# Kernel tuning notes

Hardware: AMD Instinct MI355X
Metric: run time of the kernel (lower is better)

## Reference

```python
import jax, jax.numpy as jnp
import numpy as np

B, S, DIM = 2, 2048, 1024
N_HEAD, HEAD_DIM = 16, 64


def setup_inputs() -> dict:
    key = jax.random.key(0)
    k1, k2, k3, k4 = jax.random.split(key, 4)
    x = jax.random.normal(k1, (B, S, DIM), dtype=jnp.float32)
    # rotary table: cos/sin pairs, shape [S, head_dim//2, 2]
    half = HEAD_DIM // 2
    inv_freq = 1.0 / (10000.0 ** (jnp.arange(0, half, dtype=jnp.float32) / half))
    t = jnp.arange(S, dtype=jnp.float32)
    ang = t[:, None] * inv_freq[None, :]
    freqs_cis = jnp.stack([jnp.cos(ang), jnp.sin(ang)], axis=-1)  # [S, half, 2]
    # causal boolean mask [1,1,S,S] (True = attend)
    mask = jnp.tril(jnp.ones((S, S), dtype=bool))[None, None]
    wqkv = jax.random.normal(k2, (3 * DIM, DIM), dtype=jnp.float32) * (DIM ** -0.5)
    wo = jax.random.normal(k3, (DIM, DIM), dtype=jnp.float32) * (DIM ** -0.5)
    return {"x": x, "freqs_cis": freqs_cis, "mask": mask, "wqkv": wqkv, "wo": wo}


def apply_rotary_emb(x, freqs_cis):
    # x: [B, S, H, D]; freqs_cis: [S, D//2, 2]
    xs = x.reshape(*x.shape[:-1], -1, 2)  # [B,S,H,D//2,2]
    fc = freqs_cis[None, :, None, :, :]  # [1,S,1,D//2,2]
    xr, xi = xs[..., 0], xs[..., 1]
    cr, ci = fc[..., 0], fc[..., 1]
    out = jnp.stack([xr * cr - xi * ci, xi * cr + xr * ci], axis=-1)
    return out.reshape(x.shape)


def reference(x, freqs_cis, mask, wqkv, wo):
    bsz, seqlen, _ = x.shape
    qkv = jnp.einsum('bsd,ed->bse', x, wqkv)  # [B,S,3*dim]
    q, k, v = jnp.split(qkv, 3, axis=-1)
    q = q.reshape(bsz, seqlen, N_HEAD, HEAD_DIM)
    k = k.reshape(bsz, seqlen, N_HEAD, HEAD_DIM)
    v = v.reshape(bsz, seqlen, N_HEAD, HEAD_DIM)
    q = apply_rotary_emb(q, freqs_cis)
    k = apply_rotary_emb(k, freqs_cis)
    scale = HEAD_DIM ** -0.5
    scores = jnp.einsum('bqhd,bkhd->bhqk', q, k) * scale  # [B,H,S,S]
    scores = jnp.where(mask, scores, jnp.finfo(scores.dtype).min)
    attn = jax.nn.softmax(scores, axis=-1)
    y = jnp.einsum('bhqk,bkhd->bqhd', attn, v).reshape(bsz, seqlen, N_HEAD * HEAD_DIM)
    return jnp.einsum('bse,de->bsd', y, wo)
```

## Files before the change

kernel.cpp:

```cpp
#include <hip/hip_runtime.h>
#include <hip/hip_bf16.h>
#include <stdint.h>


typedef __attribute__((ext_vector_type(8))) __bf16 bf16x8;
typedef __attribute__((ext_vector_type(4))) float f32x4;
typedef __attribute__((ext_vector_type(16))) float f32x16;

union B8 { uint4 u; bf16x8 v; unsigned short us[8]; };

static __device__ __forceinline__ float bf2f(unsigned short u) {
  union { unsigned int ui; float f; } x; x.ui = ((unsigned int)u) << 16; return x.f;
}
static __device__ __forceinline__ unsigned short f2bf(float f) {
  union { float f; unsigned int ui; } x; x.f = f;
  unsigned int r = x.ui + 0x7fffu + ((x.ui >> 16) & 1u);
  return (unsigned short)(r >> 16);
}
static __device__ __forceinline__ unsigned int cvt_pk_bf16(float lo, float hi) {
  unsigned int r;
  asm("v_cvt_pk_bf16_f32 %0, %1, %2" : "=v"(r) : "v"(lo), "v"(hi));
  return r;
}
static __device__ __forceinline__ f32x4 mfma16(bf16x8 a, bf16x8 b, f32x4 c) {
  return __builtin_amdgcn_mfma_f32_16x16x32_bf16(a, b, c, 0, 0, 0);
}
static __device__ __forceinline__ f32x16 mfma32(bf16x8 a, bf16x8 b, f32x16 c) {
  return __builtin_amdgcn_mfma_f32_32x32x16_bf16(a, b, c, 0, 0, 0);
}
#define AS1 __attribute__((address_space(1)))
#define AS3 __attribute__((address_space(3)))
static __device__ __forceinline__ void gload_lds16(const void* g, void* l) {
  __builtin_amdgcn_global_load_lds((const AS1 unsigned int*)g,
                                   (AS3 unsigned int*)l, 16, 0, 0);
}
#define VM_WAIT(N) do { \
    asm volatile("s_waitcnt vmcnt(" #N ")" ::: "memory"); \
    __builtin_amdgcn_sched_barrier(0); } while (0)
#define SBAR() __builtin_amdgcn_s_barrier()

__global__ __launch_bounds__(256) void cvt_all_kernel(
    const float* __restrict__ x, const float* __restrict__ wqkv,
    const float* __restrict__ wo,
    unsigned short* __restrict__ xb, unsigned short* __restrict__ wqkvb,
    unsigned short* __restrict__ wob) {
  int i = blockIdx.x * 256 + threadIdx.x;
  const float* src; unsigned short* dst; int off;
  if (i < 1048576)       { src = x;    dst = xb;    off = i; }
  else if (i < 1835008)  { src = wqkv; dst = wqkvb; off = i - 1048576; }
  else                   { src = wo;   dst = wob;   off = i - 1835008; }
  float4 f = ((const float4*)src)[off];
  ushort4 u;
  u.x = f2bf(f.x); u.y = f2bf(f.y); u.z = f2bf(f.z); u.w = f2bf(f.w);
  ((ushort4*)dst)[off] = u;
}

__global__ __launch_bounds__(512) void qkv_rope_kernel(
    const unsigned short* __restrict__ xb,
    const unsigned short* __restrict__ wqkvb,
    const float* __restrict__ freqs,
    unsigned short* __restrict__ Q,
    unsigned short* __restrict__ K,
    unsigned short* __restrict__ Vt)
{
  __shared__ __align__(16) unsigned short As[2][256 * 64];
  __shared__ __align__(16) unsigned short Bs[2][192 * 64];
  const int t = threadIdx.x;
  const int lane = t & 63, wv = t >> 6;
  const int l31 = lane & 31, lh = lane >> 5;
  const int wm = wv >> 1, wn = wv & 1;
  const int blk = blockIdx.x;
  const int xcd = blk & 7, j = blk >> 3;
  const int tm = 2 * xcd + (j >> 4), tn = j & 15;
  const int m0 = tm * 256, n0 = tn * 192;

  f32x16 acc[2][3] = {};

  auto stage = [&](int bb, int k0) {
    for (int r = 0; r < 7; ++r) {
      int cid = t + 512 * r;
      if (cid < 2048) {
        int row = cid >> 3, jc = cid & 7, sc = jc ^ (row & 7);
        gload_lds16(xb + (size_t)(m0 + row) * 1024 + k0 + sc * 8,
                    (char*)As[bb] + cid * 16);
      } else {
        int c2 = cid - 2048;
        int row = c2 >> 3, jc = c2 & 7, sc = jc ^ (row & 7);
        gload_lds16(wqkvb + (size_t)(n0 + row) * 1024 + k0 + sc * 8,
                    (char*)Bs[bb] + c2 * 16);
      }
    }
  };

  auto compute = [&](const char* Ap, const char* Bp) {
    for (int kst = 0; kst < 4; ++kst) {
      const int g = kst * 2 + lh;
      bf16x8 a[2], b[3];
      for (int sm = 0; sm < 2; ++sm) {
        int ra = wm * 64 + sm * 32 + l31;
        a[sm] = *(const bf16x8*)(Ap + ra * 128 + (g ^ (ra & 7)) * 16);
      }
      for (int sn = 0; sn < 3; ++sn) {
        int rb = wn * 96 + sn * 32 + l31;
        b[sn] = *(const bf16x8*)(Bp + rb * 128 + (g ^ (rb & 7)) * 16);
      }
      for (int sm = 0; sm < 2; ++sm)
        for (int sn = 0; sn < 3; ++sn)
          acc[sm][sn] = mfma32(a[sm], b[sn], acc[sm][sn]);
    }
  };

  stage(0, 0);
  for (int t2 = 0; t2 < 16; t2 += 2) {
    stage(1, (t2 + 1) * 64);
    VM_WAIT(7);
    SBAR();
    compute((const char*)As[0], (const char*)Bs[0]);
    SBAR();
    if (t2 < 14) { stage(0, (t2 + 2) * 64); VM_WAIT(7); }
    else         { VM_WAIT(0); }
    SBAR();
    compute((const char*)As[1], (const char*)Bs[1]);
    SBAR();
  }

  char* vbuf = (char*)As + wv * 2304;
  for (int sm = 0; sm < 2; ++sm) {
    for (int sn = 0; sn < 3; ++sn) {
      const int e0 = n0 + wn * 96 + sn * 32;
      const int seg = e0 >> 10;
      const int eh0 = e0 & 1023;
      const int h = eh0 >> 6;
      const int mB = m0 + wm * 64 + sm * 32;
      const int b_ = mB >> 11, sB = mB & 2047;
      if (seg == 2) {
        for (int rp = 0; rp < 8; ++rp) {
          const int r = rp * 2;
          const int row = (r & 3) + 8 * (r >> 2) + 4 * lh;
          unsigned int u = cvt_pk_bf16(acc[sm][sn][r], acc[sm][sn][r + 1]);
          *(unsigned int*)(vbuf + l31 * 72 + row * 2) = u;
        }
        const int dbase = eh0 & 63;
        for (int rd = 0; rd < 2; ++rd) {
          const int cc = rd * 16 + (lane >> 2);
          const int sh = lane & 3;
          uint2 lo = *(const uint2*)(vbuf + cc * 72 + sh * 16);
          uint2 hi = *(const uint2*)(vbuf + cc * 72 + sh * 16 + 8);
          uint4 w; w.x = lo.x; w.y = lo.y; w.z = hi.x; w.w = hi.y;
          *(uint4*)(Vt + ((size_t)(b_ * 16 + h) * 64 + dbase + cc) * 2048
                       + sB + sh * 8) = w;
        }
      } else {
        const int d = (e0 + l31) & 63;
        for (int r = 0; r < 16; ++r) {
          const int s_ = sB + (r & 3) + 8 * (r >> 2) + 4 * lh;
          float v = acc[sm][sn][r];
          float partner = __shfl_xor(v, 1, 64);
          float2 fc = *(const float2*)(freqs + s_ * 64 + (d & ~1));
          float outv = (d & 1) ? (v * fc.x + partner * fc.y)
                               : (v * fc.x - partner * fc.y);
          unsigned short* dst = (seg == 0) ? Q : K;
          dst[((size_t)(b_ * 16 + h) * 2048 + s_) * 64 + d] = f2bf(outv);
        }
      }
    }
  }
}

struct QState {
  bf16x8 qf0, qf1;
  f32x4 o[4];
  float lp;
};

static __device__ __forceinline__ void load_q(QState& st,
    const unsigned short* Qb, int q0, int c, int quad) {
  st.qf0 = *(const bf16x8*)(Qb + (q0 + c) * 64 + quad * 8);
  st.qf1 = *(const bf16x8*)(Qb + (q0 + c) * 64 + 32 + quad * 8);
}

static __device__ __forceinline__ void attn_chunk(
    QState& st, const char* Ks, const char* Vs, unsigned short* myp,
    int c, int quad, int k0, int q0, bool diag)
{
  f32x4 sfr[4];
  __builtin_amdgcn_s_setprio(1);
  for (int kc = 0; kc < 4; ++kc) {
    const int key = kc * 16 + c;
    const int s0 = quad ^ (key & 7), s1 = (4 + quad) ^ (key & 7);
    f32x4 sacc = {};
    sacc = mfma16(*(const bf16x8*)(Ks + key * 128 + s0 * 16), st.qf0, sacc);
    sacc = mfma16(*(const bf16x8*)(Ks + key * 128 + s1 * 16), st.qf1, sacc);
    sfr[kc] = sacc;
  }
  __builtin_amdgcn_s_setprio(0);
  const int qrow = q0 + c;
  float e[4][4];
  float lsum = 0.f;
  for (int kc = 0; kc < 4; ++kc) {
    for (int i = 0; i < 4; ++i) {
      float arg = fmaf(sfr[kc][i], 0.18033688f, -20.19773057f);
      if (diag && (k0 + kc * 16 + quad * 4 + i > qrow)) arg = -1e30f;
      e[kc][i] = __builtin_amdgcn_exp2f(arg);
    }
    lsum += (e[kc][0] + e[kc][1]) + (e[kc][2] + e[kc][3]);
  }
  st.lp += lsum;
  for (int kc = 0; kc < 4; ++kc) {
    uint2 w;
    w.x = cvt_pk_bf16(e[kc][0], e[kc][1]);
    w.y = cvt_pk_bf16(e[kc][2], e[kc][3]);
    *(uint2*)(myp + c * 72 + kc * 16 + quad * 4) = w;
  }
  bf16x8 pf[2];
  pf[0] = *(const bf16x8*)(myp + c * 72 + quad * 8);
  pf[1] = *(const bf16x8*)(myp + c * 72 + 32 + quad * 8);
  __builtin_amdgcn_s_setprio(1);
  for (int ct = 0; ct < 4; ++ct) {
    const int d = ct * 16 + c;
    const int s0 = quad ^ (d & 7), s1 = (4 + quad) ^ (d & 7);
    st.o[ct] = mfma16(pf[0], *(const bf16x8*)(Vs + d * 128 + s0 * 16), st.o[ct]);
    st.o[ct] = mfma16(pf[1], *(const bf16x8*)(Vs + d * 128 + s1 * 16), st.o[ct]);
  }
  __builtin_amdgcn_s_setprio(0);
}

__global__ __launch_bounds__(256) void attn_partial_kernel(
    const unsigned short* __restrict__ Q,
    const unsigned short* __restrict__ K,
    const unsigned short* __restrict__ Vt,
    unsigned short* __restrict__ Po,
    float* __restrict__ Pl)
{
  __shared__ __align__(16) unsigned short Ks[64 * 64];
  __shared__ __align__(16) unsigned short Vs[64 * 64];
  __shared__ __align__(16) unsigned short plds[4][16 * 72];
  const int t = threadIdx.x;
  const int lane = t & 63, wv = t >> 6;
  const int c = lane & 15, quad = lane >> 4;
  const int bh = blockIdx.x & 31;
  const int rest = blockIdx.x >> 5;
  const int j = rest >> 1, half = rest & 1;
  const int qA = j * 64 + wv * 16;
  const int qB = (31 - j) * 64 + wv * 16;

  const unsigned short* Qb = Q + (size_t)bh * (2048 * 64);
  const unsigned short* Kb = K + (size_t)bh * (2048 * 64);
  const unsigned short* Vb = Vt + (size_t)bh * (64 * 2048);

  QState A = {}, Bst = {};
  load_q(A, Qb, qA, c, quad);
  load_q(Bst, Qb, qB, c, quad);

  unsigned short* myp = plds[wv];
  const int ktmax = 31 - j;

  for (int kt = half; kt <= ktmax; kt += 2) {
    const int k0 = kt * 64;
    __syncthreads();
    for (int r = 0; r < 2; ++r) {
      int cid = t + 256 * r;
      int row = cid >> 3, jc = cid & 7;
      int sc = jc ^ (row & 7);
      gload_lds16(Kb + (size_t)(k0 + row) * 64 + sc * 8, (char*)Ks + cid * 16);
      gload_lds16(Vb + (size_t)row * 2048 + k0 + sc * 8, (char*)Vs + cid * 16);
    }
    __syncthreads();
    attn_chunk(Bst, (const char*)Ks, (const char*)Vs, myp, c, quad,
               k0, qB, kt == ktmax);
    if (kt <= j)
      attn_chunk(A, (const char*)Ks, (const char*)Vs, myp, c, quad,
                 k0, qA, kt == j);
  }

  unsigned short* Poh = Po + (size_t)half * (32 * 2048 * 64) + (size_t)bh * (2048 * 64);
  float* Plh = Pl + (size_t)half * (32 * 2048) + bh * 2048;
  for (int set = 0; set < 2; ++set) {
    QState& st = set ? Bst : A;
    const int q0 = set ? qB : qA;
    float l = st.lp;
    l += __shfl_xor(l, 16, 64);
    l += __shfl_xor(l, 32, 64);
    for (int i = 0; i < 4; ++i) {
      const int s = q0 + quad * 4 + i;
      for (int ct = 0; ct < 4; ++ct)
        Poh[(size_t)s * 64 + ct * 16 + c] = f2bf(st.o[ct][i]);
    }
    if (quad == 0) Plh[q0 + c] = l;
  }
}

__global__ __launch_bounds__(256) void combine_kernel(
    const unsigned short* __restrict__ Po, const float* __restrict__ Pl,
    unsigned short* __restrict__ Yb)
{
  const int idx = blockIdx.x * 256 + threadIdx.x;
  const int bh = idx >> 14, rem = idx & 16383;
  const int s = rem >> 3, g = rem & 7;
  const size_t base = (size_t)bh * (2048 * 64) + (size_t)s * 64 + g * 8;
  B8 a, b;
  a.u = *(const uint4*)(Po + base);
  b.u = *(const uint4*)(Po + (size_t)(32 * 2048 * 64) + base);
  float l = Pl[bh * 2048 + s] + Pl[32 * 2048 + bh * 2048 + s];
  float inv = 1.0f / l;
  B8 y;
  for (int k = 0; k < 8; ++k)
    y.us[k] = f2bf((bf2f(a.us[k]) + bf2f(b.us[k])) * inv);
  const int b_ = bh >> 4, h = bh & 15;
  *(uint4*)(Yb + ((size_t)(b_ * 2048 + s)) * 1024 + h * 64 + g * 8) = y.u;
}

__global__ __launch_bounds__(256) void attn_kernel(
    const unsigned short* __restrict__ Q,
    const unsigned short* __restrict__ K,
    const unsigned short* __restrict__ Vt,
    unsigned short* __restrict__ Y)
{
  __shared__ __align__(16) unsigned short Ks[64 * 64];
  __shared__ __align__(16) unsigned short Vs[64 * 64];
  __shared__ __align__(16) unsigned short plds[4][16 * 72];
  const int t = threadIdx.x;
  const int lane = t & 63, wv = t >> 6;
  const int c = lane & 15, quad = lane >> 4;
  const int j = blockIdx.x >> 5, bh = blockIdx.x & 31;
  const int b = bh >> 4, h = bh & 15;
  const int qA = j * 64 + wv * 16;
  const int qB = (31 - j) * 64 + wv * 16;

  const unsigned short* Qb = Q + (size_t)bh * (2048 * 64);
  const unsigned short* Kb = K + (size_t)bh * (2048 * 64);
  const unsigned short* Vb = Vt + (size_t)bh * (64 * 2048);

  QState A = {}, Bst = {};
  load_q(A, Qb, qA, c, quad);
  load_q(Bst, Qb, qB, c, quad);

  const int nkt = 32 - j;
  unsigned short* myp = plds[wv];

  for (int kt = 0; kt < nkt; ++kt) {
    const int k0 = kt * 64;
    __syncthreads();
    for (int r = 0; r < 2; ++r) {
      int cid = t + 256 * r;
      int row = cid >> 3, jc = cid & 7;
      int sc = jc ^ (row & 7);
      gload_lds16(Kb + (size_t)(k0 + row) * 64 + sc * 8, (char*)Ks + cid * 16);
      gload_lds16(Vb + (size_t)row * 2048 + k0 + sc * 8, (char*)Vs + cid * 16);
    }
    __syncthreads();
    attn_chunk(Bst, (const char*)Ks, (const char*)Vs, myp, c, quad,
               k0, qB, kt == 31 - j);
    if (kt <= j)
      attn_chunk(A, (const char*)Ks, (const char*)Vs, myp, c, quad,
                 k0, qA, kt == j);
  }

  for (int set = 0; set < 2; ++set) {
    QState& st = set ? Bst : A;
    const int q0 = set ? qB : qA;
    float l = st.lp;
    l += __shfl_xor(l, 16, 64);
    l += __shfl_xor(l, 32, 64);
    for (int i = 0; i < 4; ++i) {
      float inv = 1.0f / __shfl(l, quad * 4 + i, 64);
      const int s = q0 + quad * 4 + i;
      unsigned short* dst = Y + ((size_t)(b * 2048 + s)) * 1024 + h * 64;
      for (int ct = 0; ct < 4; ++ct)
        dst[ct * 16 + c] = f2bf(st.o[ct][i] * inv);
    }
  }
}

__global__ __launch_bounds__(256) void out_proj_kernel(
    const unsigned short* __restrict__ Y,
    const unsigned short* __restrict__ wob,
    float* __restrict__ out)
{
  __shared__ __align__(16) unsigned short As[2][128 * 64];
  __shared__ __align__(16) unsigned short Bs[2][64 * 64];
  const int t = threadIdx.x;
  const int lane = t & 63, wv = t >> 6;
  const int l31 = lane & 31, lh = lane >> 5;
  const int wm = wv >> 1, wn = wv & 1;
  const int blk = blockIdx.x;
  const int tm = (blk & 7) * 4 + ((blk >> 3) & 3);
  const int tn = blk >> 5;
  const int m0 = tm * 128, n0 = tn * 64;

  f32x16 acc[2] = {};

  auto stage = [&](int bb, int k0) {
    for (int r = 0; r < 6; ++r) {
      int cid = t + 256 * r;
      if (cid < 1024) {
        int row = cid >> 3, jc = cid & 7, sc = jc ^ (row & 7);
        gload_lds16(Y + (size_t)(m0 + row) * 1024 + k0 + sc * 8,
                    (char*)As[bb] + cid * 16);
      } else {
        int c2 = cid - 1024;
        int row = c2 >> 3, jc = c2 & 7, sc = jc ^ (row & 7);
        gload_lds16(wob + (size_t)(n0 + row) * 1024 + k0 + sc * 8,
                    (char*)Bs[bb] + c2 * 16);
      }
    }
  };

  auto compute = [&](const char* Ap, const char* Bp) {
    for (int kst = 0; kst < 4; ++kst) {
      const int g = kst * 2 + lh;
      bf16x8 a[2], b;
      for (int sm = 0; sm < 2; ++sm) {
        int ra = wm * 64 + sm * 32 + l31;
        a[sm] = *(const bf16x8*)(Ap + ra * 128 + (g ^ (ra & 7)) * 16);
      }
      int rb = wn * 32 + l31;
      b = *(const bf16x8*)(Bp + rb * 128 + (g ^ (rb & 7)) * 16);
      acc[0] = mfma32(a[0], b, acc[0]);
      acc[1] = mfma32(a[1], b, acc[1]);
    }
  };

  stage(0, 0);
  for (int t2 = 0; t2 < 16; t2 += 2) {
    stage(1, (t2 + 1) * 64);
    VM_WAIT(6);
    SBAR();
    compute((const char*)As[0], (const char*)Bs[0]);
    SBAR();
    if (t2 < 14) { stage(0, (t2 + 2) * 64); VM_WAIT(6); }
    else         { VM_WAIT(0); }
    SBAR();
    compute((const char*)As[1], (const char*)Bs[1]);
    SBAR();
  }

  const int col = n0 + wn * 32 + l31;
  for (int sm = 0; sm < 2; ++sm)
    for (int r = 0; r < 16; ++r) {
      const int m = m0 + wm * 64 + sm * 32 + (r & 3) + 8 * (r >> 2) + 4 * lh;
      out[(size_t)m * 1024 + col] = acc[sm][r];
    }
}

extern "C" void kernel_launch(void* const* d_in, const int* in_sizes, int n_in,
                              void* d_out, int out_size, void* d_ws, size_t ws_size,
                              hipStream_t stream) {
  const float* x     = (const float*)d_in[0];
  const float* freqs = (const float*)d_in[1];
  const float* wqkv  = (const float*)d_in[3];
  const float* wo    = (const float*)d_in[4];
  float* out = (float*)d_out;

  const size_t BHSD = (size_t)2 * 16 * 2048 * 64;
  unsigned short* Q     = (unsigned short*)d_ws;
  unsigned short* K     = Q + BHSD;
  unsigned short* Vt    = K + BHSD;
  unsigned short* Yb    = Vt + BHSD;
  unsigned short* xb    = Yb + BHSD;
  unsigned short* wqkvb = xb + 4194304;
  unsigned short* wob   = wqkvb + 3145728;
  unsigned short* Po    = wob + 1048576;
  float*          Pl    = (float*)(Po + 2 * BHSD);

  const size_t need_fast =
      (size_t)((char*)(Pl + 2 * 32 * 2048) - (char*)d_ws);

  cvt_all_kernel<<<8192, 256, 0, stream>>>(x, wqkv, wo, xb, wqkvb, wob);
  qkv_rope_kernel<<<256, 512, 0, stream>>>(xb, wqkvb, freqs, Q, K, Vt);
  if (ws_size >= need_fast) {
    attn_partial_kernel<<<1024, 256, 0, stream>>>(Q, K, Vt, Po, Pl);
    combine_kernel<<<2048, 256, 0, stream>>>(Po, Pl, Yb);
  } else {
    attn_kernel<<<512, 256, 0, stream>>>(Q, K, Vt, Yb);
  }
  out_proj_kernel<<<512, 256, 0, stream>>>(Yb, wob, out);
}
```

Baseline: 200.9 us.

## Fuse fp32-to-bf16 conversion into GEMM staging and drop separate convert kernel

Removes the standalone conversion kernel. The QKV projection and output projection now load fp32 x, wqkv and wo directly into registers, pack them to bf16 and write them to LDS. The register-staged loads are issued before the compute of the current tile so that global latency overlaps the MFMA work. This saves one launch and the bf16 round-trip through global memory, at the cost of reading twice the bytes for weights and activations on every tile, using more registers, and giving up the direct global-to-LDS loads for those operands.

```diff
diff --git a/kernel.cpp b/kernel.cpp
--- a/kernel.cpp
+++ b/kernel.cpp
@@ -21,6 +21,12 @@
   unsigned int r;
   asm("v_cvt_pk_bf16_f32 %0, %1, %2" : "=v"(r) : "v"(lo), "v"(hi));
   return r;
+}
+static __device__ __forceinline__ uint4 pack8(float4 a, float4 b) {
+  uint4 w;
+  w.x = cvt_pk_bf16(a.x, a.y); w.y = cvt_pk_bf16(a.z, a.w);
+  w.z = cvt_pk_bf16(b.x, b.y); w.w = cvt_pk_bf16(b.z, b.w);
+  return w;
 }
 static __device__ __forceinline__ f32x4 mfma16(bf16x8 a, bf16x8 b, f32x4 c) {
   return __builtin_amdgcn_mfma_f32_16x16x32_bf16(a, b, c, 0, 0, 0);
@@ -34,30 +40,18 @@
   __builtin_amdgcn_global_load_lds((const AS1 unsigned int*)g,
                                    (AS3 unsigned int*)l, 16, 0, 0);
 }
-#define VM_WAIT(N) do { \
-    asm volatile("s_waitcnt vmcnt(" #N ")" ::: "memory"); \
+#define VM_WAIT0() do { \
+    asm volatile("s_waitcnt vmcnt(0)" ::: "memory"); \
     __builtin_amdgcn_sched_barrier(0); } while (0)
+#define LGKM_WAIT() do { \
+    asm volatile("s_waitcnt lgkmcnt(0)" ::: "memory"); \
+    __builtin_amdgcn_sched_barrier(0); } while (0)
+#define SFENCE() __builtin_amdgcn_sched_barrier(0)
 #define SBAR() __builtin_amdgcn_s_barrier()
 
-__global__ __launch_bounds__(256) void cvt_all_kernel(
-    const float* __restrict__ x, const float* __restrict__ wqkv,
-    const float* __restrict__ wo,
-    unsigned short* __restrict__ xb, unsigned short* __restrict__ wqkvb,
-    unsigned short* __restrict__ wob) {
-  int i = blockIdx.x * 256 + threadIdx.x;
-  const float* src; unsigned short* dst; int off;
-  if (i < 1048576)       { src = x;    dst = xb;    off = i; }
-  else if (i < 1835008)  { src = wqkv; dst = wqkvb; off = i - 1048576; }
-  else                   { src = wo;   dst = wob;   off = i - 1835008; }
-  float4 f = ((const float4*)src)[off];
-  ushort4 u;
-  u.x = f2bf(f.x); u.y = f2bf(f.y); u.z = f2bf(f.z); u.w = f2bf(f.w);
-  ((ushort4*)dst)[off] = u;
-}
-
 __global__ __launch_bounds__(512) void qkv_rope_kernel(
-    const unsigned short* __restrict__ xb,
-    const unsigned short* __restrict__ wqkvb,
+    const float* __restrict__ x,
+    const float* __restrict__ wqkv,
     const float* __restrict__ freqs,
     unsigned short* __restrict__ Q,
     unsigned short* __restrict__ K,
@@ -76,19 +70,30 @@
 
   f32x16 acc[2][3] = {};
 
-  auto stage = [&](int bb, int k0) {
+  auto stage_load = [&](int k0, float4* ld) {
+#pragma unroll
     for (int r = 0; r < 7; ++r) {
       int cid = t + 512 * r;
-      if (cid < 2048) {
+      const float* src;
+      if (r < 4) {
         int row = cid >> 3, jc = cid & 7, sc = jc ^ (row & 7);
-        gload_lds16(xb + (size_t)(m0 + row) * 1024 + k0 + sc * 8,
-                    (char*)As[bb] + cid * 16);
+        src = x + (size_t)(m0 + row) * 1024 + k0 + sc * 8;
       } else {
         int c2 = cid - 2048;
         int row = c2 >> 3, jc = c2 & 7, sc = jc ^ (row & 7);
-        gload_lds16(wqkvb + (size_t)(n0 + row) * 1024 + k0 + sc * 8,
-                    (char*)Bs[bb] + c2 * 16);
+        src = wqkv + (size_t)(n0 + row) * 1024 + k0 + sc * 8;
       }
+      ld[2 * r]     = ((const float4*)src)[0];
+      ld[2 * r + 1] = ((const float4*)src)[1];
+    }
+  };
+  auto stage_write = [&](int bb, const float4* ld) {
+#pragma unroll
+    for (int r = 0; r < 7; ++r) {
+      int cid = t + 512 * r;
+      char* dst = (r < 4) ? (char*)As[bb] + cid * 16
+                          : (char*)Bs[bb] + (cid - 2048) * 16;
+      *(uint4*)dst = pack8(ld[2 * r], ld[2 * r + 1]);
     }
   };
 
@@ -110,17 +115,28 @@
     }
   };
 
-  stage(0, 0);
+  float4 ld[14];
+  stage_load(0, ld);
+  VM_WAIT0();
+  stage_write(0, ld);
+  LGKM_WAIT();
+  SBAR();
   for (int t2 = 0; t2 < 16; t2 += 2) {
-    stage(1, (t2 + 1) * 64);
-    VM_WAIT(7);
+    stage_load((t2 + 1) * 64, ld);
+    SFENCE();
+    compute((const char*)As[0], (const char*)Bs[0]);
+    VM_WAIT0();
+    stage_write(1, ld);
+    LGKM_WAIT();
     SBAR();
-    compute((const char*)As[0], (const char*)Bs[0]);
-    SBAR();
-    if (t2 < 14) { stage(0, (t2 + 2) * 64); VM_WAIT(7); }
-    else         { VM_WAIT(0); }
-    SBAR();
+    if (t2 < 14) stage_load((t2 + 2) * 64, ld);
+    SFENCE();
     compute((const char*)As[1], (const char*)Bs[1]);
+    if (t2 < 14) {
+      VM_WAIT0();
+      stage_write(0, ld);
+      LGKM_WAIT();
+    }
     SBAR();
   }
 
@@ -374,7 +390,7 @@
 
 __global__ __launch_bounds__(256) void out_proj_kernel(
     const unsigned short* __restrict__ Y,
-    const unsigned short* __restrict__ wob,
+    const float* __restrict__ wo,
     float* __restrict__ out)
 {
   __shared__ __align__(16) unsigned short As[2][128 * 64];
@@ -390,19 +406,30 @@
 
   f32x16 acc[2] = {};
 
-  auto stage = [&](int bb, int k0) {
-    for (int r = 0; r < 6; ++r) {
+  auto stage_A = [&](int bb, int k0) {
+#pragma unroll
+    for (int r = 0; r < 4; ++r) {
       int cid = t + 256 * r;
-      if (cid < 1024) {
-        int row = cid >> 3, jc = cid & 7, sc = jc ^ (row & 7);
-        gload_lds16(Y + (size_t)(m0 + row) * 1024 + k0 + sc * 8,
-                    (char*)As[bb] + cid * 16);
-      } else {
-        int c2 = cid - 1024;
-        int row = c2 >> 3, jc = c2 & 7, sc = jc ^ (row & 7);
-        gload_lds16(wob + (size_t)(n0 + row) * 1024 + k0 + sc * 8,
-                    (char*)Bs[bb] + c2 * 16);
-      }
+      int row = cid >> 3, jc = cid & 7, sc = jc ^ (row & 7);
+      gload_lds16(Y + (size_t)(m0 + row) * 1024 + k0 + sc * 8,
+                  (char*)As[bb] + cid * 16);
+    }
+  };
+  auto stage_loadB = [&](int k0, float4* lb) {
+#pragma unroll
+    for (int r = 0; r < 2; ++r) {
+      int cid = t + 256 * r;
+      int row = cid >> 3, jc = cid & 7, sc = jc ^ (row & 7);
+      const float* src = wo + (size_t)(n0 + row) * 1024 + k0 + sc * 8;
+      lb[2 * r]     = ((const float4*)src)[0];
+      lb[2 * r + 1] = ((const float4*)src)[1];
+    }
+  };
+  auto stage_writeB = [&](int bb, const float4* lb) {
+#pragma unroll
+    for (int r = 0; r < 2; ++r) {
+      int cid = t + 256 * r;
+      *(uint4*)((char*)Bs[bb] + cid * 16) = pack8(lb[2 * r], lb[2 * r + 1]);
     }
   };
 
@@ -421,17 +448,30 @@
     }
   };
 
-  stage(0, 0);
+  float4 lb[4];
+  stage_A(0, 0);
+  stage_loadB(0, lb);
+  VM_WAIT0();
+  stage_writeB(0, lb);
+  LGKM_WAIT();
+  SBAR();
   for (int t2 = 0; t2 < 16; t2 += 2) {
-    stage(1, (t2 + 1) * 64);
-    VM_WAIT(6);
+    stage_A(1, (t2 + 1) * 64);
+    stage_loadB((t2 + 1) * 64, lb);
+    SFENCE();
+    compute((const char*)As[0], (const char*)Bs[0]);
+    VM_WAIT0();
+    stage_writeB(1, lb);
+    LGKM_WAIT();
     SBAR();
-    compute((const char*)As[0], (const char*)Bs[0]);
-    SBAR();
-    if (t2 < 14) { stage(0, (t2 + 2) * 64); VM_WAIT(6); }
-    else         { VM_WAIT(0); }
-    SBAR();
+    if (t2 < 14) { stage_A(0, (t2 + 2) * 64); stage_loadB((t2 + 2) * 64, lb); }
+    SFENCE();
     compute((const char*)As[1], (const char*)Bs[1]);
+    if (t2 < 14) {
+      VM_WAIT0();
+      stage_writeB(0, lb);
+      LGKM_WAIT();
+    }
     SBAR();
   }
 
@@ -466,13 +506,12 @@
   const size_t need_fast =
       (size_t)((char*)(Pl + 2 * 32 * 2048) - (char*)d_ws);
 
-  cvt_all_kernel<<<8192, 256, 0, stream>>>(x, wqkv, wo, xb, wqkvb, wob);
-  qkv_rope_kernel<<<256, 512, 0, stream>>>(xb, wqkvb, freqs, Q, K, Vt);
+  qkv_rope_kernel<<<256, 512, 0, stream>>>(x, wqkv, freqs, Q, K, Vt);
   if (ws_size >= need_fast) {
     attn_partial_kernel<<<1024, 256, 0, stream>>>(Q, K, Vt, Po, Pl);
     combine_kernel<<<2048, 256, 0, stream>>>(Po, Pl, Yb);
   } else {
     attn_kernel<<<512, 256, 0, stream>>>(Q, K, Vt, Yb);
   }
-  out_proj_kernel<<<512, 256, 0, stream>>>(Yb, wob, out);
-}
+  out_proj_kernel<<<512, 256, 0, stream>>>(Yb, wo, out);
+}
```

Result: no change. 202.3 us (+0.7%).
